# Kernel optimization log

Measured on AMD Instinct MI355X. Metric: run time of the kernel, lower is better.

Reference implementation:

```python
import jax, jax.numpy as jnp
import numpy as np


def setup_inputs() -> dict:
    key = jax.random.key(0)
    k1, k2 = jax.random.split(key)
    B, V = 1024, 128000
    logits = jax.random.normal(k1, (B, V), dtype=jnp.float32)
    labels = jax.random.randint(k2, (B,), 0, V, dtype=jnp.int64)
    return {"logits": logits, "labels": labels}


def reference(logits, labels):
    # Vocab-parallel cross-entropy collapsed to single-device math:
    # global max across all splits, exp, global exp-sum, softmax,
    # gather label probability, -log, mean over batch.
    m = jnp.max(logits, axis=1, keepdims=True)            # [B, 1] global max
    exp_logit = jnp.exp(logits - m)                       # [B, V]
    exp_sum_all = jnp.sum(exp_logit, axis=1, keepdims=True)  # [B, 1] reduce_add
    softmax = exp_logit / exp_sum_all                     # [B, V]
    B = logits.shape[0]
    label_prob = softmax[jnp.arange(B), labels]           # sparse one-hot gather
    loss = jnp.mean(-jnp.log(label_prob))
    return loss
```

## Files before the change

### kernel.cpp

```cpp
#include <hip/hip_runtime.h>
#include <math.h>


#define VOCAB 128000
#define BATCH 1024
#define TPB 256

__global__ __launch_bounds__(TPB) void ce_row_kernel(const float* __restrict__ logits,
                                                     const int* __restrict__ labels,
                                                     float* __restrict__ row_loss) {
    const int row = blockIdx.x;
    const float4* __restrict__ rp =
        reinterpret_cast<const float4*>(logits + (size_t)row * VOCAB);
    const int n4 = VOCAB / 4;

    float m = -INFINITY;
    float s = 0.0f;

    for (int i = threadIdx.x; i < n4; i += TPB) {
        float4 v = rp[i];
        float m4 = fmaxf(fmaxf(v.x, v.y), fmaxf(v.z, v.w));
        if (m4 > m) {
            s *= __expf(m - m4);
            m = m4;
        }
        s += __expf(v.x - m) + __expf(v.y - m) + __expf(v.z - m) + __expf(v.w - m);
    }

    #pragma unroll
    for (int off = 1; off < 64; off <<= 1) {
        float mo = __shfl_down(m, off);
        float so = __shfl_down(s, off);
        float mn = fmaxf(m, mo);
        s = s * __expf(m - mn) + so * __expf(mo - mn);
        m = mn;
    }

    __shared__ float sm[TPB / 64], ss[TPB / 64];
    const int wave = threadIdx.x >> 6;
    const int lane = threadIdx.x & 63;
    if (lane == 0) { sm[wave] = m; ss[wave] = s; }
    __syncthreads();

    if (threadIdx.x == 0) {
        float M = sm[0], S = ss[0];
        #pragma unroll
        for (int w = 1; w < TPB / 64; ++w) {
            float mn = fmaxf(M, sm[w]);
            S = S * __expf(M - mn) + ss[w] * __expf(sm[w] - mn);
            M = mn;
        }
        const float xl = logits[(size_t)row * VOCAB + labels[row]];
        row_loss[row] = (M - xl) + __logf(S);
    }
}

__global__ __launch_bounds__(TPB) void ce_reduce_kernel(const float* __restrict__ row_loss,
                                                        float* __restrict__ out) {
    float v = 0.0f;
    for (int i = threadIdx.x; i < BATCH; i += TPB) v += row_loss[i];
    #pragma unroll
    for (int off = 1; off < 64; off <<= 1) v += __shfl_down(v, off);

    __shared__ float sv[TPB / 64];
    if ((threadIdx.x & 63) == 0) sv[threadIdx.x >> 6] = v;
    __syncthreads();
    if (threadIdx.x == 0) {
        float t = 0.0f;
        #pragma unroll
        for (int w = 0; w < TPB / 64; ++w) t += sv[w];
        out[0] = t / (float)BATCH;
    }
}

extern "C" void kernel_launch(void* const* d_in, const int* in_sizes, int n_in,
                              void* d_out, int out_size, void* d_ws, size_t ws_size,
                              hipStream_t stream) {
    const float* logits = (const float*)d_in[0];
    const int* labels = (const int*)d_in[1];
    float* row_loss = (float*)d_ws;
    float* out = (float*)d_out;

    ce_row_kernel<<<BATCH, TPB, 0, stream>>>(logits, labels, row_loss);
    ce_reduce_kernel<<<1, TPB, 0, stream>>>(row_loss, out);
}
```

Baseline: 106.2 us.

## Split each row across multiple blocks with partial max/sum combine

Each row's vocabulary is split into five chunks, each handled by its own block that writes a partial max and exp-sum. A single-block combine kernel merges the partials per row, gathers the label logit and computes the mean loss. The goal is more blocks to fill the CUs and more memory parallelism; the online-softmax update is also made branchless and the loop unrolled. The cost is extra partial writes and more serial work in the single combine block, including 1024 scattered label-logit loads.

Result: faster. 98.14 us (-7.6%).

```diff
diff --git a/kernel.cpp b/kernel.cpp
--- a/kernel.cpp
+++ b/kernel.cpp
@@ -4,27 +4,31 @@
 
 #define VOCAB 128000
 #define BATCH 1024
+#define SPLITS 5
 #define TPB 256
+#define CHUNK4 (VOCAB / 4 / SPLITS)
 
-__global__ __launch_bounds__(TPB) void ce_row_kernel(const float* __restrict__ logits,
-                                                     const int* __restrict__ labels,
-                                                     float* __restrict__ row_loss) {
-    const int row = blockIdx.x;
+__global__ __launch_bounds__(TPB) void ce_partial_kernel(const float* __restrict__ logits,
+                                                         float* __restrict__ part_m,
+                                                         float* __restrict__ part_s) {
+    const int blk = blockIdx.x;
+    const int row = blk / SPLITS;
+    const int split = blk % SPLITS;
     const float4* __restrict__ rp =
-        reinterpret_cast<const float4*>(logits + (size_t)row * VOCAB);
-    const int n4 = VOCAB / 4;
+        reinterpret_cast<const float4*>(logits + (size_t)row * VOCAB) + split * CHUNK4;
 
     float m = -INFINITY;
     float s = 0.0f;
 
-    for (int i = threadIdx.x; i < n4; i += TPB) {
+    #pragma unroll 5
+    for (int i = threadIdx.x; i < CHUNK4; i += TPB) {
         float4 v = rp[i];
         float m4 = fmaxf(fmaxf(v.x, v.y), fmaxf(v.z, v.w));
-        if (m4 > m) {
-            s *= __expf(m - m4);
-            m = m4;
-        }
-        s += __expf(v.x - m) + __expf(v.y - m) + __expf(v.z - m) + __expf(v.w - m);
+        float mn = fmaxf(m, m4);
+        s = s * __expf(m - mn)
+            + __expf(v.x - mn) + __expf(v.y - mn)
+            + __expf(v.z - mn) + __expf(v.w - mn);
+        m = mn;
     }
 
     #pragma unroll
@@ -38,8 +42,7 @@
 
     __shared__ float sm[TPB / 64], ss[TPB / 64];
     const int wave = threadIdx.x >> 6;
-    const int lane = threadIdx.x & 63;
-    if (lane == 0) { sm[wave] = m; ss[wave] = s; }
+    if ((threadIdx.x & 63) == 0) { sm[wave] = m; ss[wave] = s; }
     __syncthreads();
 
     if (threadIdx.x == 0) {
@@ -50,20 +53,37 @@
             S = S * __expf(M - mn) + ss[w] * __expf(sm[w] - mn);
             M = mn;
         }
-        const float xl = logits[(size_t)row * VOCAB + labels[row]];
-        row_loss[row] = (M - xl) + __logf(S);
+        part_m[blk] = M;
+        part_s[blk] = S;
     }
 }
 
-__global__ __launch_bounds__(TPB) void ce_reduce_kernel(const float* __restrict__ row_loss,
-                                                        float* __restrict__ out) {
-    float v = 0.0f;
-    for (int i = threadIdx.x; i < BATCH; i += TPB) v += row_loss[i];
+__global__ __launch_bounds__(TPB) void ce_combine_kernel(const float* __restrict__ part_m,
+                                                         const float* __restrict__ part_s,
+                                                         const float* __restrict__ logits,
+                                                         const int* __restrict__ labels,
+                                                         float* __restrict__ out) {
+    float local = 0.0f;
+    for (int r = threadIdx.x; r < BATCH; r += TPB) {
+        float M = part_m[r * SPLITS];
+        float S = part_s[r * SPLITS];
+        #pragma unroll
+        for (int k = 1; k < SPLITS; ++k) {
+            float pm = part_m[r * SPLITS + k];
+            float ps = part_s[r * SPLITS + k];
+            float mn = fmaxf(M, pm);
+            S = S * __expf(M - mn) + ps * __expf(pm - mn);
+            M = mn;
+        }
+        float xl = logits[(size_t)r * VOCAB + labels[r]];
+        local += (M - xl) + __logf(S);
+    }
+
     #pragma unroll
-    for (int off = 1; off < 64; off <<= 1) v += __shfl_down(v, off);
+    for (int off = 1; off < 64; off <<= 1) local += __shfl_down(local, off);
 
     __shared__ float sv[TPB / 64];
-    if ((threadIdx.x & 63) == 0) sv[threadIdx.x >> 6] = v;
+    if ((threadIdx.x & 63) == 0) sv[threadIdx.x >> 6] = local;
     __syncthreads();
     if (threadIdx.x == 0) {
         float t = 0.0f;
@@ -78,9 +98,10 @@
                               hipStream_t stream) {
     const float* logits = (const float*)d_in[0];
     const int* labels = (const int*)d_in[1];
-    float* row_loss = (float*)d_ws;
+    float* part_m = (float*)d_ws;
+    float* part_s = (float*)d_ws + BATCH * SPLITS;
     float* out = (float*)d_out;
 
-    ce_row_kernel<<<BATCH, TPB, 0, stream>>>(logits, labels, row_loss);
-    ce_reduce_kernel<<<1, TPB, 0, stream>>>(row_loss, out);
+    ce_partial_kernel<<<BATCH * SPLITS, TPB, 0, stream>>>(logits, part_m, part_s);
+    ce_combine_kernel<<<1, TPB, 0, stream>>>(part_m, part_s, logits, labels, out);
 }
```
